# Kernel optimization log

Hardware: AMD Instinct MI355X
Metric: run time of the kernel (lower is better)

The kernel has to match this reference:

```python
import jax, jax.numpy as jnp
import numpy as np

N_PATCHES = 14
HIDDEN_D = 768
N_HEADS = 12
D_HEAD = HIDDEN_D // N_HEADS
OUT_D = 1000
IMG = 224
C = 3
PS = IMG // N_PATCHES  # 16
SEQ = N_PATCHES * N_PATCHES + 1  # 197
INPUT_D = C * PS * PS  # 768
EPS = 1e-5


def positional_embeddings(s, d):
    i = jnp.arange(s, dtype=jnp.float32)[:, None]
    j = jnp.arange(d, dtype=jnp.float32)[None, :]
    even = jnp.sin(i / jnp.power(10000.0, j / d))
    odd = jnp.cos(i / jnp.power(10000.0, (j - 1.0) / d))
    return jnp.where(jnp.arange(d)[None, :] % 2 == 0, even, odd)


def layernorm_2d(x, g, b):
    # torch nn.LayerNorm((S, D)): normalize over last two dims jointly, biased var
    mu = jnp.mean(x, axis=(-2, -1), keepdims=True)
    var = jnp.var(x, axis=(-2, -1), keepdims=True)
    return (x - mu) * jax.lax.rsqrt(var + EPS) * g + b


def setup_inputs() -> dict:
    key = jax.random.key(0)
    ks = jax.random.split(key, 16)
    s = 0.02
    return {
        "images": jax.random.normal(ks[0], (64, C, IMG, IMG), jnp.float32),
        "W_map": jax.random.normal(ks[1], (INPUT_D, HIDDEN_D), jnp.float32) * s,
        "b_map": jnp.zeros((HIDDEN_D,), jnp.float32),
        "cls_tok": jax.random.uniform(ks[2], (1, HIDDEN_D), jnp.float32),
        "ln1_g": jnp.ones((SEQ, HIDDEN_D), jnp.float32),
        "ln1_b": jnp.zeros((SEQ, HIDDEN_D), jnp.float32),
        "Wq": jax.random.normal(ks[3], (N_HEADS, D_HEAD, D_HEAD), jnp.float32) * s,
        "bq": jnp.zeros((N_HEADS, D_HEAD), jnp.float32),
        "Wk": jax.random.normal(ks[4], (N_HEADS, D_HEAD, D_HEAD), jnp.float32) * s,
        "bk": jnp.zeros((N_HEADS, D_HEAD), jnp.float32),
        "Wv": jax.random.normal(ks[5], (N_HEADS, D_HEAD, D_HEAD), jnp.float32) * s,
        "bv": jnp.zeros((N_HEADS, D_HEAD), jnp.float32),
        "ln2_g": jnp.ones((SEQ, HIDDEN_D), jnp.float32),
        "ln2_b": jnp.zeros((SEQ, HIDDEN_D), jnp.float32),
        "W_enc": jax.random.normal(ks[6], (HIDDEN_D, HIDDEN_D), jnp.float32) * s,
        "b_enc": jnp.zeros((HIDDEN_D,), jnp.float32),
        "W_out": jax.random.normal(ks[7], (HIDDEN_D, OUT_D), jnp.float32) * s,
        "b_out": jnp.zeros((OUT_D,), jnp.float32),
    }


def reference(images, W_map, b_map, cls_tok, ln1_g, ln1_b, Wq, bq, Wk, bk, Wv, bv,
              ln2_g, ln2_b, W_enc, b_enc, W_out, b_out):
    n = images.shape[0]
    # patchify: [N,C,H,W] -> [N, np*np, C*ps*ps], patch flattened in (C,ph,pw) order
    p = images.reshape(n, C, N_PATCHES, PS, N_PATCHES, PS)
    patches = p.transpose(0, 2, 4, 1, 3, 5).reshape(n, N_PATCHES * N_PATCHES, INPUT_D)

    tokens = patches @ W_map + b_map  # [N, np^2, D]
    cls = jnp.broadcast_to(cls_tok[None], (n, 1, HIDDEN_D))
    tokens = jnp.concatenate([cls, tokens], axis=1)  # [N, S, D]
    tokens = tokens + positional_embeddings(SEQ, HIDDEN_D)[None]

    # MSA on ln1(tokens), vectorized over batch and heads
    x = layernorm_2d(tokens, ln1_g, ln1_b)
    xh = x.reshape(n, SEQ, N_HEADS, D_HEAD)  # split hidden into heads
    q = jnp.einsum('bshd,hde->bshe', xh, Wq) + bq[None, None]
    k = jnp.einsum('bshd,hde->bshe', xh, Wk) + bk[None, None]
    v = jnp.einsum('bshd,hde->bshe', xh, Wv) + bv[None, None]
    scores = jnp.einsum('bshe,bthe->bhst', q, k) / np.sqrt(D_HEAD).astype(np.float32)
    attn = jax.nn.softmax(scores, axis=-1)  # [B,H,S,S]
    msa = jnp.einsum('bhst,bthe->bshe', attn, v).reshape(n, SEQ, HIDDEN_D)

    out = tokens + msa
    out = out + jax.nn.relu(layernorm_2d(out, ln2_g, ln2_b) @ W_enc + b_enc)
    cls_out = out[:, 0]  # [N, D]
    return jax.nn.softmax(cls_out @ W_out + b_out, axis=-1)
```

## Files before the change

### kernel.cpp

```cpp
#include <hip/hip_runtime.h>
#include <math.h>

#define SEQL 197
#define HD 768
#define NH 12
#define DHD 64
#define BATCH 64
#define OUTD 1000

typedef unsigned short ushort_t;
typedef __attribute__((ext_vector_type(8))) short bf16x8;
typedef __attribute__((ext_vector_type(4))) float f32x4;

static __device__ __forceinline__ unsigned short f2bf(float f) {
    union { float f; unsigned u; } v; v.f = f;
    unsigned r = v.u + 0x7fff + ((v.u >> 16) & 1);
    return (unsigned short)(r >> 16);
}

static __device__ __forceinline__ void gload16(const ushort_t* g, ushort_t* l) {
    __builtin_amdgcn_global_load_lds(
        (const __attribute__((address_space(1))) unsigned int*)g,
        (__attribute__((address_space(3))) unsigned int*)l, 16, 0, 0);
}

static __device__ __forceinline__ int xcd_chunk(int id, int nwg) {
    int xcd = id & 7, ii = id >> 3;
    int q = nwg >> 3, r = nwg & 7;
    return (xcd < r) ? (xcd * (q + 1) + ii) : (r * (q + 1) + (xcd - r) * q + ii);
}

__global__ void k_init(const float* __restrict__ cls_tok, float* __restrict__ pos,
                       float* __restrict__ tok, float* __restrict__ stats) {
    int i = blockIdx.x * 256 + threadIdx.x;
    if (i < SEQL * HD) {
        int s = i / HD, d = i % HD;
        float f = (float)(d & ~1);
        float r = powf(10000.0f, -f / (float)HD);
        float a = (float)s * r;
        pos[i] = (d & 1) ? cosf(a) : sinf(a);
    } else {
        int j = i - SEQL * HD;
        if (j < BATCH * HD) {
            int b = j / HD, e = j % HD;
            float v = cls_tok[e] + ((e & 1) ? 1.0f : 0.0f);
            tok[(b * SEQL) * HD + e] = v;
            float sv = v, qv = v * v;
#pragma unroll
            for (int off = 32; off > 0; off >>= 1) {
                sv += __shfl_down(sv, off);
                qv += __shfl_down(qv, off);
            }
            if ((threadIdx.x & 63) == 0) {
                atomicAdd(&stats[2 * b], sv);
                atomicAdd(&stats[2 * b + 1], qv);
            }
        }
    }
}

__global__ void k_cvtAll(const float* __restrict__ W_map, const float* __restrict__ W_enc,
                         const float* __restrict__ Wq, const float* __restrict__ Wk,
                         const float* __restrict__ Wv,
                         ushort_t* __restrict__ WmT, ushort_t* __restrict__ WeT,
                         ushort_t* __restrict__ wt, float* __restrict__ stats,
                         float* __restrict__ logits) {
    int idx = blockIdx.x * 256 + threadIdx.x;
    if (blockIdx.x == 0 && threadIdx.x < 256) stats[threadIdx.x] = 0.f;
    if (idx < BATCH * OUTD) logits[idx] = 0.f;
    if (idx < 2 * 147456) {
        const float* W = (idx < 147456) ? W_map : W_enc;
        ushort_t* WT   = (idx < 147456) ? WmT : WeT;
        int i = (idx < 147456) ? idx : idx - 147456;
        int k = i / 192, nq = i % 192;
        float4 w = *(const float4*)&W[k * 768 + nq * 4];
        WT[(nq * 4 + 0) * 768 + k] = f2bf(w.x);
        WT[(nq * 4 + 1) * 768 + k] = f2bf(w.y);
        WT[(nq * 4 + 2) * 768 + k] = f2bf(w.z);
        WT[(nq * 4 + 3) * 768 + k] = f2bf(w.w);
    } else {
        int i = idx - 2 * 147456;
        if (i < 36864) {
            int dq = i & 15;
            int e  = (i >> 4) & 63;
            int h  = (i >> 10) % 12;
            int pj = i / 12288;
            const float* W = (pj == 0) ? Wq : (pj == 1) ? Wk : Wv;
            ushort4 o;
            o.x = f2bf(W[(h * 64 + dq * 4 + 0) * 64 + e]);
            o.y = f2bf(W[(h * 64 + dq * 4 + 1) * 64 + e]);
            o.z = f2bf(W[(h * 64 + dq * 4 + 2) * 64 + e]);
            o.w = f2bf(W[(h * 64 + dq * 4 + 3) * 64 + e]);
            *(ushort4*)&wt[(size_t)((pj * 12 + h) * 64 + e) * 64 + dq * 4] = o;
        }
    }
}

__global__ void k_prep_patches(const float* __restrict__ img, ushort_t* __restrict__ Ae) {
    int idx = blockIdx.x * 256 + threadIdx.x;
    int m = idx / 192, kq = idx % 192;
    int k0 = kq * 4;
    int c = k0 >> 8, rem = k0 & 255, ir = rem >> 4, jc = rem & 15;
    int b = m / 196, pi = m % 196;
    int pr = pi / 14, pc = pi % 14;
    float4 v = *(const float4*)&img[((b * 3 + c) * 224 + pr * 16 + ir) * 224 + pc * 16 + jc];
    ushort4 o;
    o.x = f2bf(v.x); o.y = f2bf(v.y); o.z = f2bf(v.z); o.w = f2bf(v.w);
    *(ushort4*)&Ae[m * 768 + k0] = o;
}

template <int MODE>
__launch_bounds__(256)
__global__ void k_gemm_bf16(const ushort_t* __restrict__ A, const ushort_t* __restrict__ Bt,
                            const float* __restrict__ bias, const float* __restrict__ pos,
                            float* __restrict__ out, int Mtot, float* __restrict__ stats,
                            int nwg) {
    __shared__ ushort_t As[128 * 64];
    __shared__ ushort_t Bs[128 * 64];
    __shared__ float redS[4][4];
    const int vid = xcd_chunk(blockIdx.x, nwg);
    const int m0 = (vid / 6) * 128;
    const int n0 = (vid % 6) * 128;
    const int tid = threadIdx.x;
    const int lane = tid & 63, wave = tid >> 6;
    const int wm = wave >> 1, wn = wave & 1;

    f32x4 acc[4][4];
#pragma unroll
    for (int i = 0; i < 4; ++i)
#pragma unroll
        for (int j = 0; j < 4; ++j)
#pragma unroll
            for (int r = 0; r < 4; ++r) acc[i][j][r] = 0.f;

    for (int kt = 0; kt < 12; ++kt) {
        const int k0 = kt * 64;
#pragma unroll
        for (int t = 0; t < 4; ++t) {
            int c = (wave << 2) | t;
            int o = c * 1024 + lane * 16;
            int row = o >> 7;
            int inner = o & 127;
            int col = (inner ^ ((row & 7) << 4)) >> 1;
            gload16(&A[(size_t)(m0 + row) * 768 + k0 + col], &As[c * 512]);
            gload16(&Bt[(size_t)(n0 + row) * 768 + k0 + col], &Bs[c * 512]);
        }
        __syncthreads();
#pragma unroll
        for (int ks = 0; ks < 2; ++ks) {
            const int cbyte = ks * 64 + (lane >> 4) * 16;
            bf16x8 af[4], bf[4];
#pragma unroll
            for (int mi = 0; mi < 4; ++mi) {
                int row = wm * 64 + mi * 16 + (lane & 15);
                af[mi] = *(const bf16x8*)((const char*)As + row * 128 + (cbyte ^ ((row & 7) << 4)));
            }
#pragma unroll
            for (int ni = 0; ni < 4; ++ni) {
                int n = wn * 64 + ni * 16 + (lane & 15);
                bf[ni] = *(const bf16x8*)((const char*)Bs + n * 128 + (cbyte ^ ((n & 7) << 4)));
            }
#pragma unroll
            for (int mi = 0; mi < 4; ++mi)
#pragma unroll
                for (int ni = 0; ni < 4; ++ni)
                    acc[mi][ni] = __builtin_amdgcn_mfma_f32_16x16x32_bf16(af[mi], bf[ni], acc[mi][ni], 0, 0, 0);
        }
        __syncthreads();
    }

    const int colb = n0 + wn * 64 + (lane & 15);
    const int rowb = m0 + wm * 64 + (lane >> 4) * 4;
    float s_lo = 0.f, q_lo = 0.f, s_hi = 0.f, q_hi = 0.f;
    const int bA = m0 / 196;
    const int mSplit = (bA + 1) * 196;
#pragma unroll
    for (int ni = 0; ni < 4; ++ni) {
        const int n = colb + ni * 16;
        const float bn = bias[n];
#pragma unroll
        for (int mi = 0; mi < 4; ++mi) {
#pragma unroll
            for (int r = 0; r < 4; ++r) {
                int m = rowb + mi * 16 + r;
                if (MODE == 0) {
                    int b = m / 196, s = 1 + m % 196;
                    float oval = acc[mi][ni][r] + bn + pos[s * HD + n];
                    out[((b * SEQL) + s) * HD + n] = oval;
                    if (m < mSplit) { s_lo += oval; q_lo += oval * oval; }
                    else            { s_hi += oval; q_hi += oval * oval; }
                } else {
                    if (m < Mtot) {
                        float* p = &out[(size_t)m * HD + n];
                        *p = *p + fmaxf(acc[mi][ni][r] + bn, 0.f);
                    }
                }
            }
        }
    }
    if (MODE == 0) {
#pragma unroll
        for (int off = 32; off > 0; off >>= 1) {
            s_lo += __shfl_down(s_lo, off);
            q_lo += __shfl_down(q_lo, off);
            s_hi += __shfl_down(s_hi, off);
            q_hi += __shfl_down(q_hi, off);
        }
        if (lane == 0) {
            redS[wave][0] = s_lo; redS[wave][1] = q_lo;
            redS[wave][2] = s_hi; redS[wave][3] = q_hi;
        }
        __syncthreads();
        if (tid == 0) {
            float a0 = 0.f, a1 = 0.f, a2 = 0.f, a3 = 0.f;
#pragma unroll
            for (int i = 0; i < 4; ++i) {
                a0 += redS[i][0]; a1 += redS[i][1];
                a2 += redS[i][2]; a3 += redS[i][3];
            }
            atomicAdd(&stats[2 * bA], a0);
            atomicAdd(&stats[2 * bA + 1], a1);
            int bB = bA + 1;
            if (bB < BATCH) {
                atomicAdd(&stats[2 * bB], a2);
                atomicAdd(&stats[2 * bB + 1], a3);
            }
        }
    }
}

__launch_bounds__(512, 2)
__global__ void k_qkvattn(const float* __restrict__ tok, float* __restrict__ stats,
                          const float* __restrict__ g1, const float* __restrict__ b1,
                          const ushort_t* __restrict__ wt,
                          const float* __restrict__ bq, const float* __restrict__ bk,
                          const float* __restrict__ bv, float* __restrict__ out) {
    const int vid = xcd_chunk(blockIdx.x, 768);
    const int h = vid % 12, b = vid / 12;
    __shared__ __attribute__((aligned(16))) ushort_t sm[32768];
    __shared__ float rS[8], rS2[8];
    const int tid = threadIdx.x;
    const int wave = tid >> 6, lane = tid & 63;
    const int l16 = lane & 15, l4 = lane >> 4;
    const int r0 = wave * 32;
    const float inv_n = 1.0f / (float)(SEQL * HD);
    const float S1_ = stats[b * 2], S2_ = stats[b * 2 + 1];
    const float mu = S1_ * inv_n;
    const float rsg = rsqrtf(S2_ * inv_n - mu * mu + 1e-5f);
    ushort_t* A16 = sm;
    ushort_t* B16 = sm + 16384;

    {
        const int row = tid >> 1, hw = tid & 1;
        if (row < SEQL) {
            const float* tp = &tok[((size_t)b * SEQL + row) * HD + h * 64 + hw * 32];
            const float* gp = &g1[(size_t)row * HD + h * 64 + hw * 32];
            const float* bp = &b1[(size_t)row * HD + h * 64 + hw * 32];
#pragma unroll
            for (int g = 0; g < 4; ++g) {
                float4 t0 = *(const float4*)&tp[g * 8];
                float4 t1 = *(const float4*)&tp[g * 8 + 4];
                float4 ga = *(const float4*)&gp[g * 8];
                float4 gb = *(const float4*)&gp[g * 8 + 4];
                float4 ba = *(const float4*)&bp[g * 8];
                float4 bb = *(const float4*)&bp[g * 8 + 4];
                bf16x8 o;
                o[0] = (short)f2bf((t0.x - mu) * rsg * ga.x + ba.x);
                o[1] = (short)f2bf((t0.y - mu) * rsg * ga.y + ba.y);
                o[2] = (short)f2bf((t0.z - mu) * rsg * ga.z + ba.z);
                o[3] = (short)f2bf((t0.w - mu) * rsg * ga.w + ba.w);
                o[4] = (short)f2bf((t1.x - mu) * rsg * gb.x + bb.x);
                o[5] = (short)f2bf((t1.y - mu) * rsg * gb.y + bb.y);
                o[6] = (short)f2bf((t1.z - mu) * rsg * gb.z + bb.z);
                o[7] = (short)f2bf((t1.w - mu) * rsg * gb.w + bb.w);
                int pc = (hw * 32 + g * 8) ^ ((row & 7) << 3);
                *(bf16x8*)&A16[row * 64 + pc] = o;
            }
        } else {
            bf16x8 z;
#pragma unroll
            for (int j = 0; j < 8; ++j) z[j] = 0;
#pragma unroll
            for (int g = 0; g < 4; ++g) {
                int pc = (hw * 32 + g * 8) ^ ((row & 7) << 3);
                *(bf16x8*)&A16[row * 64 + pc] = z;
            }
        }
    }

    bf16x8 af[2][2];
#pragma unroll
    for (int mi = 0; mi < 2; ++mi)
#pragma unroll
        for (int kk = 0; kk < 2; ++kk) {
            int row = r0 + mi * 16 + l16;
            af[mi][kk] = *(const bf16x8*)&A16[row * 64 + ((kk * 32 + l4 * 8) ^ ((row & 7) << 3))];
        }

#define PROJ_ACC(PJ, ACC)                                                                      \
    {                                                                                          \
        _Pragma("unroll") for (int ni = 0; ni < 4; ++ni) {                                     \
            const ushort_t* wr = &wt[(size_t)(((PJ) * 12 + h) * 64 + ni * 16 + l16) * 64];     \
            bf16x8 w0 = *(const bf16x8*)&wr[l4 * 8];                                           \
            bf16x8 w1 = *(const bf16x8*)&wr[32 + l4 * 8];                                      \
            _Pragma("unroll") for (int mi = 0; mi < 2; ++mi) {                                 \
                ACC[mi][ni] = __builtin_amdgcn_mfma_f32_16x16x32_bf16(af[mi][0], w0, ACC[mi][ni], 0, 0, 0); \
                ACC[mi][ni] = __builtin_amdgcn_mfma_f32_16x16x32_bf16(af[mi][1], w1, ACC[mi][ni], 0, 0, 0); \
            }                                                                                  \
        }                                                                                      \
    }

    f32x4 acc[2][4];
#define ZERO_ACC                                                                               \
    _Pragma("unroll") for (int mi = 0; mi < 2; ++mi)                                           \
        _Pragma("unroll") for (int ni = 0; ni < 4; ++ni) {                                     \
            acc[mi][ni][0] = 0.f; acc[mi][ni][1] = 0.f; acc[mi][ni][2] = 0.f; acc[mi][ni][3] = 0.f; }

    ZERO_ACC;
    PROJ_ACC(0, acc);
#pragma unroll
    for (int ni = 0; ni < 4; ++ni) {
        float bn = bq[h * 64 + ni * 16 + l16];
#pragma unroll
        for (int mi = 0; mi < 2; ++mi)
#pragma unroll
            for (int r = 0; r < 4; ++r) {
                int row = r0 + mi * 16 + l4 * 4 + r;
                A16[row * 64 + ((ni * 16 + l16) ^ ((row & 7) << 3))] = f2bf(acc[mi][ni][r] + bn);
            }
    }
    bf16x8 qa[2][2];
#pragma unroll
    for (int mi = 0; mi < 2; ++mi)
#pragma unroll
        for (int kk = 0; kk < 2; ++kk) {
            int row = r0 + mi * 16 + l16;
            qa[mi][kk] = *(const bf16x8*)&A16[row * 64 + ((kk * 32 + l4 * 8) ^ ((row & 7) << 3))];
        }

    ZERO_ACC;
    PROJ_ACC(1, acc);
#pragma unroll
    for (int ni = 0; ni < 4; ++ni) {
        float bn = bk[h * 64 + ni * 16 + l16];
#pragma unroll
        for (int mi = 0; mi < 2; ++mi)
#pragma unroll
            for (int r = 0; r < 4; ++r) {
                int t = r0 + mi * 16 + l4 * 4 + r;
                A16[t * 64 + ((ni * 16 + l16) ^ ((t & 7) << 3))] = f2bf(acc[mi][ni][r] + bn);
            }
    }

    ZERO_ACC;
    PROJ_ACC(2, acc);
#pragma unroll
    for (int ni = 0; ni < 4; ++ni) {
        float bn = bv[h * 64 + ni * 16 + l16];
#pragma unroll
        for (int mi = 0; mi < 2; ++mi) {
            int t4 = r0 + mi * 16 + l4 * 4;
            int e = ni * 16 + l16;
            ushort4 pkt;
            pkt.x = f2bf(acc[mi][ni][0] + bn);
            pkt.y = f2bf(acc[mi][ni][1] + bn);
            pkt.z = f2bf(acc[mi][ni][2] + bn);
            pkt.w = f2bf(acc[mi][ni][3] + bn);
            *(ushort4*)&B16[e * 256 + (t4 ^ ((e & 7) << 3))] = pkt;
        }
    }

    __syncthreads();

    f32x4 sa[2][16];
#pragma unroll
    for (int ni = 0; ni < 16; ++ni) {
        int t = ni * 16 + l16;
        bf16x8 k0 = *(const bf16x8*)&A16[t * 64 + ((l4 * 8) ^ ((t & 7) << 3))];
        bf16x8 k1 = *(const bf16x8*)&A16[t * 64 + ((32 + l4 * 8) ^ ((t & 7) << 3))];
#pragma unroll
        for (int mi = 0; mi < 2; ++mi) {
            f32x4 z;
            z[0] = 0.f; z[1] = 0.f; z[2] = 0.f; z[3] = 0.f;
            z = __builtin_amdgcn_mfma_f32_16x16x32_bf16(qa[mi][0], k0, z, 0, 0, 0);
            sa[mi][ni] = __builtin_amdgcn_mfma_f32_16x16x32_bf16(qa[mi][1], k1, z, 0, 0, 0);
        }
    }

    float l_s[2][4];
#pragma unroll
    for (int mi = 0; mi < 2; ++mi)
#pragma unroll
        for (int r = 0; r < 4; ++r) {
            float rsum = 0.f;
#pragma unroll
            for (int ni = 0; ni < 16; ++ni) {
                float p = (ni * 16 + l16 < SEQL) ? __expf(sa[mi][ni][r] * 0.125f) : 0.f;
                sa[mi][ni][r] = p;
                rsum += p;
            }
            rsum += __shfl_xor(rsum, 1);
            rsum += __shfl_xor(rsum, 2);
            rsum += __shfl_xor(rsum, 4);
            rsum += __shfl_xor(rsum, 8);
            l_s[mi][r] = rsum;
        }

    __syncthreads();

    f32x4 oacc[2][4];
#pragma unroll
    for (int mi = 0; mi < 2; ++mi)
#pragma unroll
        for (int ne = 0; ne < 4; ++ne) {
            oacc[mi][ne][0] = 0.f; oacc[mi][ne][1] = 0.f;
            oacc[mi][ne][2] = 0.f; oacc[mi][ne][3] = 0.f;
        }

    for (int c = 0; c < 4; ++c) {
#pragma unroll
        for (int j = 0; j < 4; ++j)
#pragma unroll
            for (int mi = 0; mi < 2; ++mi)
#pragma unroll
                for (int r = 0; r < 4; ++r) {
                    int row = r0 + mi * 16 + l4 * 4 + r;
                    A16[row * 64 + ((j * 16 + l16) ^ ((row & 7) << 3))] = f2bf(sa[mi][c * 4 + j][r]);
                }
        bf16x8 pa[2][2];
#pragma unroll
        for (int mi = 0; mi < 2; ++mi)
#pragma unroll
            for (int kk = 0; kk < 2; ++kk) {
                int row = r0 + mi * 16 + l16;
                pa[mi][kk] = *(const bf16x8*)&A16[row * 64 + ((kk * 32 + l4 * 8) ^ ((row & 7) << 3))];
            }
#pragma unroll
        for (int ne = 0; ne < 4; ++ne) {
            int e = ne * 16 + l16;
            bf16x8 v0 = *(const bf16x8*)&B16[e * 256 + ((c * 64 + l4 * 8) ^ ((e & 7) << 3))];
            bf16x8 v1 = *(const bf16x8*)&B16[e * 256 + ((c * 64 + 32 + l4 * 8) ^ ((e & 7) << 3))];
#pragma unroll
            for (int mi = 0; mi < 2; ++mi) {
                oacc[mi][ne] = __builtin_amdgcn_mfma_f32_16x16x32_bf16(pa[mi][0], v0, oacc[mi][ne], 0, 0, 0);
                oacc[mi][ne] = __builtin_amdgcn_mfma_f32_16x16x32_bf16(pa[mi][1], v1, oacc[mi][ne], 0, 0, 0);
            }
        }
    }

    __syncthreads();
    float* Osm = (float*)sm + wave * 2048;
#pragma unroll
    for (int mi = 0; mi < 2; ++mi)
#pragma unroll
        for (int r = 0; r < 4; ++r) {
            float inv = 1.0f / l_s[mi][r];
            int rl = mi * 16 + l4 * 4 + r;
#pragma unroll
            for (int ne = 0; ne < 4; ++ne)
                Osm[rl * 64 + ((ne * 16 + l16) ^ ((rl & 3) << 4))] = oacc[mi][ne][r] * inv;
        }
    float psum = 0.f, psq = 0.f;
#pragma unroll
    for (int it = 0; it < 8; ++it) {
        int rl = it * 4 + l4;
        int row = r0 + rl;
        if (row < SEQL) {
            size_t off = ((size_t)b * SEQL + row) * HD + h * 64 + l16 * 4;
            float4 ov = *(float4*)&Osm[rl * 64 + ((l16 * 4) ^ ((rl & 3) << 4))];
            float4 tv = *(const float4*)&tok[off];
            float4 o;
            o.x = ov.x + tv.x; o.y = ov.y + tv.y;
            o.z = ov.z + tv.z; o.w = ov.w + tv.w;
            *(float4*)&out[off] = o;
            psum += o.x + o.y + o.z + o.w;
            psq  += o.x * o.x + o.y * o.y + o.z * o.z + o.w * o.w;
        }
    }
#pragma unroll
    for (int off = 32; off > 0; off >>= 1) {
        psum += __shfl_down(psum, off);
        psq += __shfl_down(psq, off);
    }
    if (lane == 0) { rS[wave] = psum; rS2[wave] = psq; }
    __syncthreads();
    if (tid == 0) {
        float S = 0.f, S2 = 0.f;
#pragma unroll
        for (int i = 0; i < 8; ++i) { S += rS[i]; S2 += rS2[i]; }
        atomicAdd(&stats[128 + 2 * b], S);
        atomicAdd(&stats[129 + 2 * b], S2);
    }
#undef PROJ_ACC
#undef ZERO_ACC
}

__global__ void k_ln2apply(const float* __restrict__ outb, const float* __restrict__ stats,
                           const float* __restrict__ g2, const float* __restrict__ b2,
                           ushort_t* __restrict__ x) {
    int i = blockIdx.x * 256 + threadIdx.x;
    if (i >= BATCH * SEQL * HD / 4) return;
    int e4 = i * 4;
    int m = e4 / HD, kk = e4 % HD;
    int b = m / SEQL, s = m % SEQL;
    const float inv_n = 1.0f / (float)(SEQL * HD);
    float S = stats[128 + 2 * b], S2 = stats[129 + 2 * b];
    float mu = S * inv_n;
    float rsg = rsqrtf(S2 * inv_n - mu * mu + 1e-5f);
    float4 t = *(const float4*)&outb[e4];
    float4 g = *(const float4*)&g2[s * HD + kk];
    float4 bb = *(const float4*)&b2[s * HD + kk];
    ushort4 o;
    o.x = f2bf((t.x - mu) * rsg * g.x + bb.x);
    o.y = f2bf((t.y - mu) * rsg * g.y + bb.y);
    o.z = f2bf((t.z - mu) * rsg * g.z + bb.z);
    o.w = f2bf((t.w - mu) * rsg * g.w + bb.w);
    *(ushort4*)&x[e4] = o;
}

__launch_bounds__(256)
__global__ void k_logits(const float* __restrict__ out, const float* __restrict__ Wo,
                         float* __restrict__ logits) {
    const int eg = blockIdx.x, b = blockIdx.y, tid = threadIdx.x;
    __shared__ float cls[192];
    if (tid < 48)
        *(float4*)&cls[tid * 4] = *(const float4*)&out[(size_t)(b * SEQL) * HD + eg * 192 + tid * 4];
    __syncthreads();
    const int o0 = tid * 4;
    if (o0 < OUTD) {
        float4 acc = {0.f, 0.f, 0.f, 0.f};
        const float* wbase = &Wo[(size_t)eg * 192 * OUTD + o0];
#pragma unroll 4
        for (int e = 0; e < 192; ++e) {
            float c = cls[e];
            float4 w = *(const float4*)&wbase[(size_t)e * OUTD];
            acc.x += c * w.x;
            acc.y += c * w.y;
            acc.z += c * w.z;
            acc.w += c * w.w;
        }
        atomicAdd(&logits[b * OUTD + o0 + 0], acc.x);
        atomicAdd(&logits[b * OUTD + o0 + 1], acc.y);
        atomicAdd(&logits[b * OUTD + o0 + 2], acc.z);
        atomicAdd(&logits[b * OUTD + o0 + 3], acc.w);
    }
}

__launch_bounds__(256)
__global__ void k_head_sm(const float* __restrict__ logits, const float* __restrict__ bo,
                          float* __restrict__ dout) {
    const int b = blockIdx.x, tid = threadIdx.x;
    __shared__ float red[256];
    const int o0 = tid * 4;
    const bool ok = (o0 < OUTD);
    float4 acc = {0.f, 0.f, 0.f, 0.f};
    if (ok) {
        float4 lg = *(const float4*)&logits[b * OUTD + o0];
        float4 bb = *(const float4*)&bo[o0];
        acc.x = lg.x + bb.x; acc.y = lg.y + bb.y;
        acc.z = lg.z + bb.z; acc.w = lg.w + bb.w;
    }
    float mx = ok ? fmaxf(fmaxf(acc.x, acc.y), fmaxf(acc.z, acc.w)) : -INFINITY;
    red[tid] = mx;
    __syncthreads();
    for (int s = 128; s > 0; s >>= 1) {
        if (tid < s) red[tid] = fmaxf(red[tid], red[tid + s]);
        __syncthreads();
    }
    float M = red[0];
    __syncthreads();
    float4 p = {0.f, 0.f, 0.f, 0.f};
    float ls = 0.f;
    if (ok) {
        p.x = expf(acc.x - M);
        p.y = expf(acc.y - M);
        p.z = expf(acc.z - M);
        p.w = expf(acc.w - M);
        ls = p.x + p.y + p.z + p.w;
    }
    red[tid] = ls;
    __syncthreads();
    for (int s = 128; s > 0; s >>= 1) {
        if (tid < s) red[tid] += red[tid + s];
        __syncthreads();
    }
    float inv = 1.0f / red[0];
    if (ok) {
        p.x *= inv; p.y *= inv; p.z *= inv; p.w *= inv;
        *(float4*)&dout[b * OUTD + o0] = p;
    }
}

extern "C" void kernel_launch(void* const* d_in, const int* in_sizes, int n_in,
                              void* d_out, int out_size, void* d_ws, size_t ws_size,
                              hipStream_t stream) {
    const float* images  = (const float*)d_in[0];
    const float* W_map   = (const float*)d_in[1];
    const float* b_map   = (const float*)d_in[2];
    const float* cls_tok = (const float*)d_in[3];
    const float* ln1_g   = (const float*)d_in[4];
    const float* ln1_b   = (const float*)d_in[5];
    const float* Wq      = (const float*)d_in[6];
    const float* bq      = (const float*)d_in[7];
    const float* Wk      = (const float*)d_in[8];
    const float* bk      = (const float*)d_in[9];
    const float* Wv      = (const float*)d_in[10];
    const float* bv      = (const float*)d_in[11];
    const float* ln2_g   = (const float*)d_in[12];
    const float* ln2_b   = (const float*)d_in[13];
    const float* W_enc   = (const float*)d_in[14];
    const float* b_enc   = (const float*)d_in[15];
    const float* W_out   = (const float*)d_in[16];
    const float* b_out   = (const float*)d_in[17];

    float* ws = (float*)d_ws;
    const size_t BIG = (size_t)BATCH * SEQL * HD;

    float* pos   = ws;
    float* tok   = ws + 151552;
    float* outb  = tok + BIG;
    float* stats = outb + BIG;
    ushort_t* wtq = (ushort_t*)(stats + 256);
    ushort_t* Ae  = wtq + 147456;
    ushort_t* WmT = Ae + (size_t)12672 * 768;
    ushort_t* WeT = WmT + (size_t)768 * 768;
    float* logits = (float*)(WeT + (size_t)768 * 768);
    ushort_t* Ae2 = Ae;

    k_cvtAll<<<1296, 256, 0, stream>>>(W_map, W_enc, Wq, Wk, Wv, WmT, WeT, wtq, stats, logits);
    k_init<<<783, 256, 0, stream>>>(cls_tok, pos, tok, stats);
    k_prep_patches<<<9408, 256, 0, stream>>>(images, Ae);
    k_gemm_bf16<0><<<588, 256, 0, stream>>>(Ae, WmT, b_map, pos, tok, 12544, stats, 588);
    k_qkvattn<<<768, 512, 0, stream>>>(tok, stats, ln1_g, ln1_b, wtq, bq, bk, bv, outb);
    k_ln2apply<<<9456, 256, 0, stream>>>(outb, stats, ln2_g, ln2_b, Ae2);
    k_gemm_bf16<1><<<594, 256, 0, stream>>>(Ae2, WeT, b_enc, pos, outb, 12608, stats, 594);
    k_logits<<<dim3(4, 64), 256, 0, stream>>>(outb, W_out, logits);
    k_head_sm<<<64, 256, 0, stream>>>(logits, b_out, (float*)d_out);
}
```

Measured before the change: 244.4 us.

## Merge three prep kernels into one launch and drop atomics for CLS stats

```diff
diff --git a/kernel.cpp b/kernel.cpp
--- a/kernel.cpp
+++ b/kernel.cpp
@@ -30,83 +30,96 @@
     return (xcd < r) ? (xcd * (q + 1) + ii) : (r * (q + 1) + (xcd - r) * q + ii);
 }
 
-__global__ void k_init(const float* __restrict__ cls_tok, float* __restrict__ pos,
-                       float* __restrict__ tok, float* __restrict__ stats) {
-    int i = blockIdx.x * 256 + threadIdx.x;
-    if (i < SEQL * HD) {
-        int s = i / HD, d = i % HD;
-        float f = (float)(d & ~1);
-        float r = powf(10000.0f, -f / (float)HD);
-        float a = (float)s * r;
-        pos[i] = (d & 1) ? cosf(a) : sinf(a);
+#define NB_CVT  1296
+#define NB_INIT 783
+__global__ void k_prep(const float* __restrict__ W_map, const float* __restrict__ W_enc,
+                       const float* __restrict__ Wq, const float* __restrict__ Wk,
+                       const float* __restrict__ Wv, const float* __restrict__ cls_tok,
+                       const float* __restrict__ img,
+                       ushort_t* __restrict__ WmT, ushort_t* __restrict__ WeT,
+                       ushort_t* __restrict__ wt, float* __restrict__ stats,
+                       float* __restrict__ logits, float* __restrict__ pos,
+                       float* __restrict__ tok, ushort_t* __restrict__ Ae) {
+    const int bx = blockIdx.x, tid = threadIdx.x;
+    if (bx < NB_CVT) {
+        int idx = bx * 256 + tid;
+        if (bx == 0) { stats[tid] = 0.f; }
+        if (idx < BATCH * OUTD) logits[idx] = 0.f;
+        if (idx < 2 * 147456) {
+            const float* W = (idx < 147456) ? W_map : W_enc;
+            ushort_t* WT   = (idx < 147456) ? WmT : WeT;
+            int i = (idx < 147456) ? idx : idx - 147456;
+            int k = i / 192, nq = i % 192;
+            float4 w = *(const float4*)&W[k * 768 + nq * 4];
+            WT[(nq * 4 + 0) * 768 + k] = f2bf(w.x);
+            WT[(nq * 4 + 1) * 768 + k] = f2bf(w.y);
+            WT[(nq * 4 + 2) * 768 + k] = f2bf(w.z);
+            WT[(nq * 4 + 3) * 768 + k] = f2bf(w.w);
+        } else {
+            int i = idx - 2 * 147456;
+            if (i < 36864) {
+                int dq = i & 15;
+                int e  = (i >> 4) & 63;
+                int h  = (i >> 10) % 12;
+                int pj = i / 12288;
+                const float* W = (pj == 0) ? Wq : (pj == 1) ? Wk : Wv;
+                ushort4 o;
+                o.x = f2bf(W[(h * 64 + dq * 4 + 0) * 64 + e]);
+                o.y = f2bf(W[(h * 64 + dq * 4 + 1) * 64 + e]);
+                o.z = f2bf(W[(h * 64 + dq * 4 + 2) * 64 + e]);
+                o.w = f2bf(W[(h * 64 + dq * 4 + 3) * 64 + e]);
+                *(ushort4*)&wt[(size_t)((pj * 12 + h) * 64 + e) * 64 + dq * 4] = o;
+            }
+        }
+    } else if (bx < NB_CVT + NB_INIT) {
+        int i = (bx - NB_CVT) * 256 + tid;
+        if (i < SEQL * HD) {
+            int s = i / HD, d = i % HD;
+            float f = (float)(d & ~1);
+            float r = powf(10000.0f, -f / (float)HD);
+            float a = (float)s * r;
+            pos[i] = (d & 1) ? cosf(a) : sinf(a);
+        } else {
+            int j = i - SEQL * HD;
+            int b = j / HD, e = j % HD;
+            tok[(b * SEQL) * HD + e] = cls_tok[e] + ((e & 1) ? 1.0f : 0.0f);
+        }
+    } else if (bx == NB_CVT + NB_INIT) {
+        __shared__ float rs[4], rs2[4];
+        float s = 0.f, s2 = 0.f;
+#pragma unroll
+        for (int j = 0; j < 3; ++j) {
+            int e = tid * 3 + j;
+            float v = cls_tok[e] + ((e & 1) ? 1.0f : 0.0f);
+            s += v; s2 += v * v;
+        }
+#pragma unroll
+        for (int off = 32; off > 0; off >>= 1) {
+            s += __shfl_down(s, off);
+            s2 += __shfl_down(s2, off);
+        }
+        int lane = tid & 63, w = tid >> 6;
+        if (lane == 0) { rs[w] = s; rs2[w] = s2; }
+        __syncthreads();
+        if (tid == 0) {
+            float S = 0.f, S2 = 0.f;
+#pragma unroll
+            for (int i = 0; i < 4; ++i) { S += rs[i]; S2 += rs2[i]; }
+            stats[256] = S;
+            stats[257] = S2;
+        }
     } else {
-        int j = i - SEQL * HD;
-        if (j < BATCH * HD) {
-            int b = j / HD, e = j % HD;
-            float v = cls_tok[e] + ((e & 1) ? 1.0f : 0.0f);
-            tok[(b * SEQL) * HD + e] = v;
-            float sv = v, qv = v * v;
-#pragma unroll
-            for (int off = 32; off > 0; off >>= 1) {
-                sv += __shfl_down(sv, off);
-                qv += __shfl_down(qv, off);
-            }
-            if ((threadIdx.x & 63) == 0) {
-                atomicAdd(&stats[2 * b], sv);
-                atomicAdd(&stats[2 * b + 1], qv);
-            }
-        }
-    }
-}
-
-__global__ void k_cvtAll(const float* __restrict__ W_map, const float* __restrict__ W_enc,
-                         const float* __restrict__ Wq, const float* __restrict__ Wk,
-                         const float* __restrict__ Wv,
-                         ushort_t* __restrict__ WmT, ushort_t* __restrict__ WeT,
-                         ushort_t* __restrict__ wt, float* __restrict__ stats,
-                         float* __restrict__ logits) {
-    int idx = blockIdx.x * 256 + threadIdx.x;
-    if (blockIdx.x == 0 && threadIdx.x < 256) stats[threadIdx.x] = 0.f;
-    if (idx < BATCH * OUTD) logits[idx] = 0.f;
-    if (idx < 2 * 147456) {
-        const float* W = (idx < 147456) ? W_map : W_enc;
-        ushort_t* WT   = (idx < 147456) ? WmT : WeT;
-        int i = (idx < 147456) ? idx : idx - 147456;
-        int k = i / 192, nq = i % 192;
-        float4 w = *(const float4*)&W[k * 768 + nq * 4];
-        WT[(nq * 4 + 0) * 768 + k] = f2bf(w.x);
-        WT[(nq * 4 + 1) * 768 + k] = f2bf(w.y);
-        WT[(nq * 4 + 2) * 768 + k] = f2bf(w.z);
-        WT[(nq * 4 + 3) * 768 + k] = f2bf(w.w);
-    } else {
-        int i = idx - 2 * 147456;
-        if (i < 36864) {
-            int dq = i & 15;
-            int e  = (i >> 4) & 63;
-            int h  = (i >> 10) % 12;
-            int pj = i / 12288;
-            const float* W = (pj == 0) ? Wq : (pj == 1) ? Wk : Wv;
-            ushort4 o;
-            o.x = f2bf(W[(h * 64 + dq * 4 + 0) * 64 + e]);
-            o.y = f2bf(W[(h * 64 + dq * 4 + 1) * 64 + e]);
-            o.z = f2bf(W[(h * 64 + dq * 4 + 2) * 64 + e]);
-            o.w = f2bf(W[(h * 64 + dq * 4 + 3) * 64 + e]);
-            *(ushort4*)&wt[(size_t)((pj * 12 + h) * 64 + e) * 64 + dq * 4] = o;
-        }
-    }
-}
-
-__global__ void k_prep_patches(const float* __restrict__ img, ushort_t* __restrict__ Ae) {
-    int idx = blockIdx.x * 256 + threadIdx.x;
-    int m = idx / 192, kq = idx % 192;
-    int k0 = kq * 4;
-    int c = k0 >> 8, rem = k0 & 255, ir = rem >> 4, jc = rem & 15;
-    int b = m / 196, pi = m % 196;
-    int pr = pi / 14, pc = pi % 14;
-    float4 v = *(const float4*)&img[((b * 3 + c) * 224 + pr * 16 + ir) * 224 + pc * 16 + jc];
-    ushort4 o;
-    o.x = f2bf(v.x); o.y = f2bf(v.y); o.z = f2bf(v.z); o.w = f2bf(v.w);
-    *(ushort4*)&Ae[m * 768 + k0] = o;
+        int idx = (bx - (NB_CVT + NB_INIT + 1)) * 256 + tid;
+        int m = idx / 192, kq = idx % 192;
+        int k0 = kq * 4;
+        int c = k0 >> 8, rem = k0 & 255, ir = rem >> 4, jc = rem & 15;
+        int b = m / 196, pi = m % 196;
+        int pr = pi / 14, pc = pi % 14;
+        float4 v = *(const float4*)&img[((b * 3 + c) * 224 + pr * 16 + ir) * 224 + pc * 16 + jc];
+        ushort4 o;
+        o.x = f2bf(v.x); o.y = f2bf(v.y); o.z = f2bf(v.z); o.w = f2bf(v.w);
+        *(ushort4*)&Ae[m * 768 + k0] = o;
+    }
 }
 
 template <int MODE>
@@ -235,8 +248,7 @@
                           const ushort_t* __restrict__ wt,
                           const float* __restrict__ bq, const float* __restrict__ bk,
                           const float* __restrict__ bv, float* __restrict__ out) {
-    const int vid = xcd_chunk(blockIdx.x, 768);
-    const int h = vid % 12, b = vid / 12;
+    const int h = blockIdx.x, b = blockIdx.y;
     __shared__ __attribute__((aligned(16))) ushort_t sm[32768];
     __shared__ float rS[8], rS2[8];
     const int tid = threadIdx.x;
@@ -244,7 +256,8 @@
     const int l16 = lane & 15, l4 = lane >> 4;
     const int r0 = wave * 32;
     const float inv_n = 1.0f / (float)(SEQL * HD);
-    const float S1_ = stats[b * 2], S2_ = stats[b * 2 + 1];
+    const float S1_ = stats[b * 2] + stats[256];
+    const float S2_ = stats[b * 2 + 1] + stats[257];
     const float mu = S1_ * inv_n;
     const float rsg = rsqrtf(S2_ * inv_n - mu * mu + 1e-5f);
     ushort_t* A16 = sm;
@@ -620,18 +633,17 @@
     float* tok   = ws + 151552;
     float* outb  = tok + BIG;
     float* stats = outb + BIG;
-    ushort_t* wtq = (ushort_t*)(stats + 256);
+    ushort_t* wtq = (ushort_t*)(stats + 512);
     ushort_t* Ae  = wtq + 147456;
     ushort_t* WmT = Ae + (size_t)12672 * 768;
     ushort_t* WeT = WmT + (size_t)768 * 768;
     float* logits = (float*)(WeT + (size_t)768 * 768);
     ushort_t* Ae2 = Ae;
 
-    k_cvtAll<<<1296, 256, 0, stream>>>(W_map, W_enc, Wq, Wk, Wv, WmT, WeT, wtq, stats, logits);
-    k_init<<<783, 256, 0, stream>>>(cls_tok, pos, tok, stats);
-    k_prep_patches<<<9408, 256, 0, stream>>>(images, Ae);
+    k_prep<<<11488, 256, 0, stream>>>(W_map, W_enc, Wq, Wk, Wv, cls_tok, images,
+                                      WmT, WeT, wtq, stats, logits, pos, tok, Ae);
     k_gemm_bf16<0><<<588, 256, 0, stream>>>(Ae, WmT, b_map, pos, tok, 12544, stats, 588);
-    k_qkvattn<<<768, 512, 0, stream>>>(tok, stats, ln1_g, ln1_b, wtq, bq, bk, bv, outb);
+    k_qkvattn<<<dim3(12, 64), 512, 0, stream>>>(tok, stats, ln1_g, ln1_b, wtq, bq, bk, bv, outb);
     k_ln2apply<<<9456, 256, 0, stream>>>(outb, stats, ln2_g, ln2_b, Ae2);
     k_gemm_bf16<1><<<594, 256, 0, stream>>>(Ae2, WeT, b_enc, pos, outb, 12608, stats, 594);
     k_logits<<<dim3(4, 64), 256, 0, stream>>>(outb, W_out, logits);
```

Result: faster. 233.8 us (-4.3%).
